# Kernel optimization log

Measured on AMD Instinct MI355X. Metric: run time of the kernel, lower is better.

## Reference

```python
import jax, jax.numpy as jnp
import numpy as np

B, S, D = 2, 2048, 4096
H, KVH, HD = 32, 8, 128          # n_heads, n_kv_heads, head_dim
N_REP = H // KVH                 # GQA repeat factor
ROPE_THETA = 10000.0
NEG = -1e9                       # finite stand-in for -inf additive mask


def setup_inputs() -> dict:
    key = jax.random.key(0)
    ks = jax.random.split(key, 5)
    x = jax.random.normal(ks[0], (B, S, D), jnp.float32)
    wq = jax.random.normal(ks[1], (D, H * HD), jnp.float32) * 0.02
    wk = jax.random.normal(ks[2], (D, KVH * HD), jnp.float32) * 0.02
    wv = jax.random.normal(ks[3], (D, KVH * HD), jnp.float32) * 0.02
    wo = jax.random.normal(ks[4], (D, D), jnp.float32) * 0.02
    # rotary frequencies: freq_cis[t, j] = exp(i * t * theta^(-2j/HD))
    inv_freq = 1.0 / (ROPE_THETA ** (jnp.arange(0, HD, 2, dtype=jnp.float32) / HD))
    angles = jnp.arange(S, dtype=jnp.float32)[:, None] * inv_freq[None, :]  # [S, HD/2]
    cos, sin = jnp.cos(angles), jnp.sin(angles)
    # causal additive mask [S, S]
    i = jnp.arange(S)
    mask = jnp.where(i[None, :] > i[:, None], NEG, 0.0).astype(jnp.float32)
    return {"x": x, "cos": cos, "sin": sin, "mask": mask,
            "wq": wq, "wk": wk, "wv": wv, "wo": wo, "start_pos": 0}


def _apply_rope(t, cos, sin):
    # t: [B, S, nH, HD] -> rotate consecutive pairs, matching view_as_complex semantics
    tp = t.reshape(*t.shape[:-1], HD // 2, 2)
    t0, t1 = tp[..., 0], tp[..., 1]
    c = cos[None, :, None, :]  # [1, S, 1, HD/2]
    s = sin[None, :, None, :]
    o0 = t0 * c - t1 * s
    o1 = t0 * s + t1 * c
    return jnp.stack([o0, o1], axis=-1).reshape(t.shape)


def reference(x, cos, sin, mask, wq, wk, wv, wo, start_pos):
    bs, seq_len, _ = x.shape
    q = (x @ wq).reshape(bs, seq_len, H, HD)
    k = (x @ wk).reshape(bs, seq_len, KVH, HD)
    v = (x @ wv).reshape(bs, seq_len, KVH, HD)
    q = _apply_rope(q, cos, sin)
    k = _apply_rope(k, cos, sin)
    # start_pos == 0 full prefill: KV cache slice [:, :start_pos+seq_len] == k, v
    # GQA: repeat_interleave kv heads (each kv head repeated N_REP times consecutively)
    k = jnp.repeat(k, N_REP, axis=2)  # [B, S, H, HD]
    v = jnp.repeat(v, N_REP, axis=2)
    attn = jnp.einsum('bqhd,bkhd->bhqk', q, k) / jnp.sqrt(jnp.float32(HD))
    attn = attn + mask[None, None, :, :]
    p = jax.nn.softmax(attn.astype(jnp.float32), axis=-1).astype(q.dtype)
    out = jnp.einsum('bhqk,bkhd->bqhd', p, v).reshape(bs, seq_len, D)
    return out @ wo
```

## Files before the change

kernel.cpp:

```cpp
#include <hip/hip_runtime.h>
#include <stdint.h>

typedef unsigned short u16;
typedef __attribute__((ext_vector_type(8))) short bf16x8;
typedef __attribute__((ext_vector_type(4))) float f32x4;

__device__ __forceinline__ u16 f2bf(float f) {
  uint32_t x = __float_as_uint(f);
  x += 0x7fffu + ((x >> 16) & 1u);
  return (u16)(x >> 16);
}
__device__ __forceinline__ float bf2f(u16 u) {
  return __uint_as_float(((uint32_t)u) << 16);
}
__device__ __forceinline__ void gload_lds16(const void* g, void* l) {
  __builtin_amdgcn_global_load_lds(
      (const __attribute__((address_space(1))) void*)g,
      (__attribute__((address_space(3))) void*)l, 16, 0, 0);
}

__device__ __forceinline__ float rope_rot(float a, int col, int srow,
                                          const float* __restrict__ cosT,
                                          const float* __restrict__ sinT) {
  float p = __shfl_xor(a, 1, 64);
  int d = (col & 127) >> 1;
  float c = cosT[srow * 64 + d];
  float sn = sinT[srow * 64 + d];
  return (col & 1) ? (p * sn + a * c) : (a * c - p * sn);
}

__global__ __launch_bounds__(256) void cvt_kernel(const float* __restrict__ x,
                                                  u16* __restrict__ y) {
  int i = blockIdx.x * 256 + threadIdx.x;
  float4 v = ((const float4*)x)[i];
  ushort4 o = make_ushort4(f2bf(v.x), f2bf(v.y), f2bf(v.z), f2bf(v.w));
  ((ushort4*)y)[i] = o;
}

__global__ __launch_bounds__(256) void transpose_cvt(const float* __restrict__ W,
                                                     u16* __restrict__ Wt,
                                                     int Kd, int Nd) {
  __shared__ float t[32][33];
  int k0 = blockIdx.y * 32, n0 = blockIdx.x * 32;
  int tx = threadIdx.x, ty = threadIdx.y;
  #pragma unroll
  for (int i = ty; i < 32; i += 8)
    t[i][tx] = W[(size_t)(k0 + i) * Nd + n0 + tx];
  __syncthreads();
  #pragma unroll
  for (int i = ty; i < 32; i += 8)
    Wt[(size_t)(n0 + i) * Kd + k0 + tx] = f2bf(t[tx][i]);
}

__global__ __launch_bounds__(256) void gemm_kv(const u16* __restrict__ A,
                                               const u16* __restrict__ Bt,
                                               u16* __restrict__ Kout,
                                               u16* __restrict__ Vt,
                                               const float* __restrict__ cosT,
                                               const float* __restrict__ sinT) {
  const int K = 4096;
  __shared__ __attribute__((aligned(16))) u16 sA[128 * 64];
  __shared__ __attribute__((aligned(16))) u16 sB[128 * 64];
  const int tid = threadIdx.x;
  const int wave = tid >> 6, lane = tid & 63;
  const int lr = lane & 15, lq = lane >> 4;
  int lin = blockIdx.y * gridDim.x + blockIdx.x;
  int cpx = (gridDim.x * gridDim.y) >> 3;
  int swz = (lin & 7) * cpx + (lin >> 3);
  const int bm = (swz >> 4) * 128, bn = (swz & 15) * 128;
  const int wm = (wave >> 1) * 64, wn = (wave & 1) * 64;
  f32x4 acc[4][4] = {};
  for (int kt = 0; kt < K; kt += 64) {
    #pragma unroll
    for (int c = 0; c < 4; ++c) {
      int chunk = wave * 4 + c;
      int eo = chunk * 512 + lane * 8;
      int r = eo >> 6, col = eo & 63;
      gload_lds16(A + (size_t)(bm + r) * K + kt + col, sA + chunk * 512);
      gload_lds16(Bt + (size_t)(bn + r) * K + kt + col, sB + chunk * 512);
    }
    __syncthreads();
    #pragma unroll
    for (int ks = 0; ks < 2; ++ks) {
      bf16x8 af[4], bfv[4];
      #pragma unroll
      for (int i = 0; i < 4; ++i)
        af[i] = *(const bf16x8*)(sA + (wm + i * 16 + lr) * 64 + ks * 32 + lq * 8);
      #pragma unroll
      for (int j = 0; j < 4; ++j)
        bfv[j] = *(const bf16x8*)(sB + (wn + j * 16 + lr) * 64 + ks * 32 + lq * 8);
      #pragma unroll
      for (int i = 0; i < 4; ++i)
        #pragma unroll
        for (int j = 0; j < 4; ++j)
          acc[i][j] = __builtin_amdgcn_mfma_f32_16x16x32_bf16(af[i], bfv[j], acc[i][j], 0, 0, 0);
    }
    __syncthreads();
  }
  #pragma unroll
  for (int i = 0; i < 4; ++i) {
    #pragma unroll
    for (int j = 0; j < 4; ++j) {
      int colg = bn + wn + j * 16 + lr;
      if (bn < 1024) {
        #pragma unroll
        for (int r = 0; r < 4; ++r) {
          int row = bm + wm + i * 16 + lq * 4 + r;
          float o = rope_rot(acc[i][j][r], colg, row & 2047, cosT, sinT);
          Kout[(size_t)row * 1024 + colg] = f2bf(o);
        }
      } else {
        int col = colg - 1024;
        int row0 = bm + wm + i * 16 + lq * 4;
        int bb = row0 >> 11, s = row0 & 2047;
        ushort4 pk = make_ushort4(f2bf(acc[i][j][0]), f2bf(acc[i][j][1]),
                                  f2bf(acc[i][j][2]), f2bf(acc[i][j][3]));
        *(ushort4*)(Vt + ((size_t)bb * 1024 + col) * 2048 + s) = pk;
      }
    }
  }
}

template <int EPI, bool ROPE>
__global__ __launch_bounds__(512, 2) void gemm256(const u16* __restrict__ A,
                                                  const u16* __restrict__ Bt,
                                                  void* __restrict__ Cout,
                                                  int M, int N, int K,
                                                  const float* __restrict__ cosT,
                                                  const float* __restrict__ sinT,
                                                  float post) {
  __shared__ __attribute__((aligned(16))) u16 sA[3][256 * 64];
  __shared__ __attribute__((aligned(16))) u16 sB[2][256 * 64];
  const int tid = threadIdx.x;
  const int wid = tid >> 6, lane = tid & 63;
  const int lr = lane & 15, lq = lane >> 4;
  const int nbn = N >> 8;
  int lin = blockIdx.y * gridDim.x + blockIdx.x;
  int cpx = (gridDim.x * gridDim.y) >> 3;
  int swz = (lin & 7) * cpx + (lin >> 3);
  const int bm = (swz / nbn) * 256, bn = (swz % nbn) * 256;
  const int wrow = (wid >> 2) * 128, wcol = (wid & 3) * 64;
  const int NK = K >> 6;

  f32x4 acc[8][4] = {};

  auto stageA = [&](int j) {
    u16* dst = &sA[j % 3][0];
    #pragma unroll
    for (int c = 0; c < 4; ++c) {
      int e = (c * 512 + tid) * 8;
      int r = e >> 6, col = e & 63;
      gload_lds16(A + (size_t)(bm + r) * K + j * 64 + (col ^ ((r & 7) << 3)), dst + e);
    }
  };
  auto stageB = [&](int j) {
    u16* dst = &sB[j & 1][0];
    #pragma unroll
    for (int c = 0; c < 4; ++c) {
      int e = (c * 512 + tid) * 8;
      int r = e >> 6, col = e & 63;
      gload_lds16(Bt + (size_t)(bn + r) * K + j * 64 + (col ^ ((r & 7) << 3)), dst + e);
    }
  };
  auto readA = [&](bf16x8* af, const u16* a_, int ks) {
    #pragma unroll
    for (int mf = 0; mf < 8; ++mf) {
      int row = wrow + mf * 16 + lr;
      af[mf] = *(const bf16x8*)(a_ + row * 64 + ((ks * 32 + lq * 8) ^ ((row & 7) << 3)));
    }
  };
  auto readB = [&](bf16x8* bfv, const u16* b_, int ks) {
    #pragma unroll
    for (int nf = 0; nf < 4; ++nf) {
      int row = wcol + nf * 16 + lr;
      bfv[nf] = *(const bf16x8*)(b_ + row * 64 + ((ks * 32 + lq * 8) ^ ((row & 7) << 3)));
    }
  };

  bf16x8 afP[8], bfP[4], afQ[8], bfQ[4];

  stageB(0); stageA(0); stageA(1); stageB(1);
  asm volatile("s_waitcnt vmcnt(8)" ::: "memory");
  asm volatile("s_barrier" ::: "memory");
  readA(afP, sA[0], 0); readB(bfP, sB[0], 0);

  for (int j = 0; j < NK; ++j) {
    const u16* a_ = sA[j % 3];
    const u16* b_ = sB[j & 1];
    const u16* an = sA[(j + 1) % 3];
    const u16* bn = sB[(j + 1) & 1];
    readA(afQ, a_, 1); readB(bfQ, b_, 1);
    if (j + 2 < NK) stageA(j + 2);
    asm volatile("s_waitcnt lgkmcnt(12)" ::: "memory");
    __builtin_amdgcn_sched_barrier(0);
    __builtin_amdgcn_s_setprio(1);
    #pragma unroll
    for (int mf = 0; mf < 8; ++mf)
      #pragma unroll
      for (int nf = 0; nf < 4; ++nf)
        acc[mf][nf] = __builtin_amdgcn_mfma_f32_16x16x32_bf16(afP[mf], bfP[nf],
                                                              acc[mf][nf], 0, 0, 0);
    __builtin_amdgcn_s_setprio(0);
    if (j + 2 < NK) asm volatile("s_waitcnt vmcnt(4)" ::: "memory");
    else            asm volatile("s_waitcnt vmcnt(0)" ::: "memory");
    asm volatile("s_barrier" ::: "memory");
    readA(afP, an, 0); readB(bfP, bn, 0);
    if (j + 2 < NK) stageB(j + 2);
    asm volatile("s_waitcnt lgkmcnt(12)" ::: "memory");
    __builtin_amdgcn_sched_barrier(0);
    __builtin_amdgcn_s_setprio(1);
    #pragma unroll
    for (int mf = 0; mf < 8; ++mf)
      #pragma unroll
      for (int nf = 0; nf < 4; ++nf)
        acc[mf][nf] = __builtin_amdgcn_mfma_f32_16x16x32_bf16(afQ[mf], bfQ[nf],
                                                              acc[mf][nf], 0, 0, 0);
    __builtin_amdgcn_s_setprio(0);
  }

  #pragma unroll
  for (int mf = 0; mf < 8; ++mf) {
    #pragma unroll
    for (int nf = 0; nf < 4; ++nf) {
      #pragma unroll
      for (int r = 0; r < 4; ++r) {
        int row = bm + wrow + mf * 16 + lq * 4 + r;
        int col = bn + wcol + nf * 16 + lr;
        if (ROPE) {
          float o = rope_rot(acc[mf][nf][r], col, row & 2047, cosT, sinT);
          ((u16*)Cout)[(size_t)row * N + col] = f2bf(o * post);
        } else if (EPI == 0) {
          ((u16*)Cout)[(size_t)row * N + col] = f2bf(acc[mf][nf][r]);
        } else {
          ((float*)Cout)[(size_t)row * N + col] = acc[mf][nf][r];
        }
      }
    }
  }
}

__global__ __launch_bounds__(256, 2) void attn_kernel(const u16* __restrict__ Q,
                                                      const u16* __restrict__ Kb,
                                                      const u16* __restrict__ Vt,
                                                      u16* __restrict__ O) {
  __shared__ __attribute__((aligned(16))) u16 sK[2][64 * 128];
  __shared__ __attribute__((aligned(16))) u16 sV[2][128 * 64];
  __shared__ __attribute__((aligned(16))) u16 sP[4][16 * 66];
  const int tid = threadIdx.x;
  const int wave = tid >> 6, lane = tid & 63;
  const int lr = lane & 15, lq = lane >> 4;
  const int p = blockIdx.x & 15;
  const int h = (blockIdx.x >> 4) & 31;
  const int b = blockIdx.x >> 9;
  const int kvh = h >> 2;
  const int qtA = p, qtB = 31 - p;
  const int q0A = qtA * 64 + wave * 16;
  const int q0B = qtB * 64 + wave * 16;
  const float NOFF = -8.0f;

  bf16x8 qfA[4], qfB[4];
  {
    const u16* qa = Q + (size_t)(b * 2048 + q0A + lr) * 4096 + h * 128 + lq * 8;
    const u16* qb = Q + (size_t)(b * 2048 + q0B + lr) * 4096 + h * 128 + lq * 8;
    #pragma unroll
    for (int ks = 0; ks < 4; ++ks) {
      qfA[ks] = *(const bf16x8*)(qa + ks * 32);
      qfB[ks] = *(const bf16x8*)(qb + ks * 32);
    }
  }

  const u16* kbase = Kb + (size_t)b * 2048 * 1024 + kvh * 128;
  const u16* vbase = Vt + (size_t)(b * 1024 + kvh * 128) * 2048;

  auto stage = [&](int kt, int bsel) {
    #pragma unroll
    for (int c = 0; c < 4; ++c) {
      int chunk = wave * 4 + c;
      int eo = chunk * 512 + lane * 8;
      int rk = eo >> 7, ck = eo & 127;
      int cks = ck ^ ((rk & 7) << 3);
      gload_lds16(kbase + (size_t)(kt * 64 + rk) * 1024 + cks,
                  (u16*)sK[bsel] + chunk * 512);
      int rv = eo >> 6, cv = eo & 63;
      int cvs = cv ^ ((rv & 7) << 3);
      gload_lds16(vbase + (size_t)rv * 2048 + kt * 64 + cvs,
                  (u16*)sV[bsel] + chunk * 512);
    }
  };

  f32x4 oA[8] = {}, oB[8] = {};
  float lA[4] = {0.f, 0.f, 0.f, 0.f}, lB[4] = {0.f, 0.f, 0.f, 0.f};

  stage(0, 0);
  __syncthreads();
  int buf = 0;
  for (int kt = 0; kt <= qtB; ++kt) {
    if (kt < qtB) stage(kt + 1, buf ^ 1);
    const u16* kb_ = sK[buf];
    const u16* vb_ = sV[buf];
    const bool doA = (kt <= qtA);

    f32x4 sAacc[4], sBacc[4];
    #pragma unroll
    for (int nf = 0; nf < 4; ++nf) {
      sAacc[nf] = (f32x4){NOFF, NOFF, NOFF, NOFF};
      sBacc[nf] = (f32x4){NOFF, NOFF, NOFF, NOFF};
    }
    __builtin_amdgcn_s_setprio(1);
    #pragma unroll
    for (int ks = 0; ks < 4; ++ks) {
      bf16x8 kf[4];
      #pragma unroll
      for (int nf = 0; nf < 4; ++nf) {
        int row = nf * 16 + lr;
        kf[nf] = *(const bf16x8*)(kb_ + row * 128 + ((ks * 32 + lq * 8) ^ ((row & 7) << 3)));
      }
      #pragma unroll
      for (int nf = 0; nf < 4; ++nf)
        sBacc[nf] = __builtin_amdgcn_mfma_f32_16x16x32_bf16(qfB[ks], kf[nf], sBacc[nf], 0, 0, 0);
      if (doA) {
        #pragma unroll
        for (int nf = 0; nf < 4; ++nf)
          sAacc[nf] = __builtin_amdgcn_mfma_f32_16x16x32_bf16(qfA[ks], kf[nf], sAacc[nf], 0, 0, 0);
      }
    }
    __builtin_amdgcn_s_setprio(0);

    auto sm_pv = [&](f32x4* sacc, float* lsum, f32x4* o, int qt, int q0) {
      float ls[4] = {0.f, 0.f, 0.f, 0.f};
      const bool diag = (kt == qt);
      #pragma unroll
      for (int nf = 0; nf < 4; ++nf)
        #pragma unroll
        for (int r = 0; r < 4; ++r) {
          float pv = __expf(sacc[nf][r]);
          if (diag) {
            int j = kt * 64 + nf * 16 + lr;
            int iq = q0 + lq * 4 + r;
            if (j > iq) pv = 0.f;
          }
          ls[r] += pv;
          sP[wave][(lq * 4 + r) * 66 + nf * 16 + lr] = f2bf(pv);
        }
      #pragma unroll
      for (int r = 0; r < 4; ++r) lsum[r] += ls[r];
      __builtin_amdgcn_s_setprio(1);
      #pragma unroll
      for (int ks = 0; ks < 2; ++ks) {
        bf16x8 pa = *(const bf16x8*)(&sP[wave][lr * 66 + ks * 32 + lq * 8]);
        #pragma unroll
        for (int df = 0; df < 8; ++df) {
          int row = df * 16 + lr;
          bf16x8 vb = *(const bf16x8*)(vb_ + row * 64 + ((ks * 32 + lq * 8) ^ ((row & 7) << 3)));
          o[df] = __builtin_amdgcn_mfma_f32_16x16x32_bf16(pa, vb, o[df], 0, 0, 0);
        }
      }
      __builtin_amdgcn_s_setprio(0);
    };

    if (doA) sm_pv(sAacc, lA, oA, qtA, q0A);
    sm_pv(sBacc, lB, oB, qtB, q0B);

    __syncthreads();
    buf ^= 1;
  }

  #pragma unroll
  for (int r = 0; r < 4; ++r) {
    float tA = lA[r], tB = lB[r];
    tA += __shfl_xor(tA, 1, 64); tB += __shfl_xor(tB, 1, 64);
    tA += __shfl_xor(tA, 2, 64); tB += __shfl_xor(tB, 2, 64);
    tA += __shfl_xor(tA, 4, 64); tB += __shfl_xor(tB, 4, 64);
    tA += __shfl_xor(tA, 8, 64); tB += __shfl_xor(tB, 8, 64);
    lA[r] = 1.f / tA; lB[r] = 1.f / tB;
  }
  #pragma unroll
  for (int df = 0; df < 8; ++df) {
    #pragma unroll
    for (int r = 0; r < 4; ++r) {
      int iqA = q0A + lq * 4 + r;
      int iqB = q0B + lq * 4 + r;
      O[(size_t)(b * 2048 + iqA) * 4096 + h * 128 + df * 16 + lr] = f2bf(oA[df][r] * lA[r]);
      O[(size_t)(b * 2048 + iqB) * 4096 + h * 128 + df * 16 + lr] = f2bf(oB[df][r] * lB[r]);
    }
  }
}

extern "C" void kernel_launch(void* const* d_in, const int* in_sizes, int n_in,
                              void* d_out, int out_size, void* d_ws, size_t ws_size,
                              hipStream_t stream) {
  (void)in_sizes; (void)n_in; (void)out_size;
  const float* x    = (const float*)d_in[0];
  const float* cosT = (const float*)d_in[1];
  const float* sinT = (const float*)d_in[2];
  const float* wq   = (const float*)d_in[4];
  const float* wk   = (const float*)d_in[5];
  const float* wv   = (const float*)d_in[6];
  const float* wo   = (const float*)d_in[7];
  float* out = (float*)d_out;
  char* ws = (char*)d_ws;

  const size_t WS_NEEDED = 201326592;
  if (ws_size < WS_NEEDED) return;

  u16* xb   = (u16*)(ws);
  u16* wqt  = (u16*)(ws + 33554432ULL);
  u16* wkvt = (u16*)(ws + 67108864ULL);
  u16* wot  = (u16*)(ws + 83886080ULL);
  u16* Qb   = (u16*)(ws + 117440512ULL);
  u16* Kbf  = (u16*)(ws + 150994944ULL);
  u16* Vt   = (u16*)(ws + 159383552ULL);
  u16* Ob   = (u16*)(ws + 167772160ULL);

  const float QSC = 0.08838834764831845f;

  cvt_kernel<<<16384, 256, 0, stream>>>(x, xb);
  transpose_cvt<<<dim3(128, 128), dim3(32, 8), 0, stream>>>(wq, wqt, 4096, 4096);
  transpose_cvt<<<dim3(32, 128),  dim3(32, 8), 0, stream>>>(wk, wkvt, 4096, 1024);
  transpose_cvt<<<dim3(32, 128),  dim3(32, 8), 0, stream>>>(wv, wkvt + 1024ULL * 4096, 4096, 1024);
  transpose_cvt<<<dim3(128, 128), dim3(32, 8), 0, stream>>>(wo, wot, 4096, 4096);

  gemm256<0, true><<<dim3(16, 16), 512, 0, stream>>>(xb, wqt, Qb, 4096, 4096, 4096,
                                                     cosT, sinT, QSC);
  gemm_kv<<<dim3(16, 32), 256, 0, stream>>>(xb, wkvt, Kbf, Vt, cosT, sinT);

  attn_kernel<<<1024, 256, 0, stream>>>(Qb, Kbf, Vt, Ob);

  gemm256<2, false><<<dim3(16, 16), 512, 0, stream>>>(Ob, wot, out, 4096, 4096, 4096,
                                                      nullptr, nullptr, 1.0f);
}
```

Before: 537.9 us.

## Software-pipeline KV GEMM with swizzled multi-buffered LDS and use exp2 softmax

Rewrites the K/V projection GEMM main loop to use a triple-buffered A and double-buffered B LDS pipeline with XOR-swizzled layout. It splits the k-tile into two halves so fragment reads for the next step overlap the MFMAs of the current one, using manual waitcnt, barrier and priority control. This is meant to hide global-load latency and LDS bank conflicts that the old single-buffer loop exposed around two syncthreads per tile. Separately, attention folds log2(e) into the Q scale and offset so the softmax can call exp2f instead of __expf. The manual vmcnt/lgkmcnt counts are fragile and raise LDS use, which may lower occupancy.

```diff
diff --git a/kernel.cpp b/kernel.cpp
--- a/kernel.cpp
+++ b/kernel.cpp
@@ -52,15 +52,16 @@
     Wt[(size_t)(n0 + i) * Kd + k0 + tx] = f2bf(t[tx][i]);
 }
 
-__global__ __launch_bounds__(256) void gemm_kv(const u16* __restrict__ A,
-                                               const u16* __restrict__ Bt,
-                                               u16* __restrict__ Kout,
-                                               u16* __restrict__ Vt,
-                                               const float* __restrict__ cosT,
-                                               const float* __restrict__ sinT) {
+__global__ __launch_bounds__(256, 2) void gemm_kv(const u16* __restrict__ A,
+                                                  const u16* __restrict__ Bt,
+                                                  u16* __restrict__ Kout,
+                                                  u16* __restrict__ Vt,
+                                                  const float* __restrict__ cosT,
+                                                  const float* __restrict__ sinT) {
   const int K = 4096;
-  __shared__ __attribute__((aligned(16))) u16 sA[128 * 64];
-  __shared__ __attribute__((aligned(16))) u16 sB[128 * 64];
+  const int NK = 64;
+  __shared__ __attribute__((aligned(16))) u16 sA[3][128 * 64];
+  __shared__ __attribute__((aligned(16))) u16 sB[2][128 * 64];
   const int tid = threadIdx.x;
   const int wave = tid >> 6, lane = tid & 63;
   const int lr = lane & 15, lq = lane >> 4;
@@ -69,34 +70,83 @@
   int swz = (lin & 7) * cpx + (lin >> 3);
   const int bm = (swz >> 4) * 128, bn = (swz & 15) * 128;
   const int wm = (wave >> 1) * 64, wn = (wave & 1) * 64;
+
   f32x4 acc[4][4] = {};
-  for (int kt = 0; kt < K; kt += 64) {
+
+  auto stageA = [&](int j) {
+    u16* dst = &sA[j % 3][0];
     #pragma unroll
     for (int c = 0; c < 4; ++c) {
-      int chunk = wave * 4 + c;
-      int eo = chunk * 512 + lane * 8;
-      int r = eo >> 6, col = eo & 63;
-      gload_lds16(A + (size_t)(bm + r) * K + kt + col, sA + chunk * 512);
-      gload_lds16(Bt + (size_t)(bn + r) * K + kt + col, sB + chunk * 512);
-    }
-    __syncthreads();
-    #pragma unroll
-    for (int ks = 0; ks < 2; ++ks) {
-      bf16x8 af[4], bfv[4];
-      #pragma unroll
-      for (int i = 0; i < 4; ++i)
-        af[i] = *(const bf16x8*)(sA + (wm + i * 16 + lr) * 64 + ks * 32 + lq * 8);
-      #pragma unroll
-      for (int j = 0; j < 4; ++j)
-        bfv[j] = *(const bf16x8*)(sB + (wn + j * 16 + lr) * 64 + ks * 32 + lq * 8);
-      #pragma unroll
-      for (int i = 0; i < 4; ++i)
-        #pragma unroll
-        for (int j = 0; j < 4; ++j)
-          acc[i][j] = __builtin_amdgcn_mfma_f32_16x16x32_bf16(af[i], bfv[j], acc[i][j], 0, 0, 0);
-    }
-    __syncthreads();
-  }
+      int e = (c * 256 + tid) * 8;
+      int r = e >> 6, col = e & 63;
+      gload_lds16(A + (size_t)(bm + r) * K + j * 64 + (col ^ ((r & 7) << 3)), dst + e);
+    }
+  };
+  auto stageB = [&](int j) {
+    u16* dst = &sB[j & 1][0];
+    #pragma unroll
+    for (int c = 0; c < 4; ++c) {
+      int e = (c * 256 + tid) * 8;
+      int r = e >> 6, col = e & 63;
+      gload_lds16(Bt + (size_t)(bn + r) * K + j * 64 + (col ^ ((r & 7) << 3)), dst + e);
+    }
+  };
+  auto readA = [&](bf16x8* af, const u16* a_, int ks) {
+    #pragma unroll
+    for (int mf = 0; mf < 4; ++mf) {
+      int row = wm + mf * 16 + lr;
+      af[mf] = *(const bf16x8*)(a_ + row * 64 + ((ks * 32 + lq * 8) ^ ((row & 7) << 3)));
+    }
+  };
+  auto readB = [&](bf16x8* bfv, const u16* b_, int ks) {
+    #pragma unroll
+    for (int nf = 0; nf < 4; ++nf) {
+      int row = wn + nf * 16 + lr;
+      bfv[nf] = *(const bf16x8*)(b_ + row * 64 + ((ks * 32 + lq * 8) ^ ((row & 7) << 3)));
+    }
+  };
+
+  bf16x8 afP[4], bfP[4], afQ[4], bfQ[4];
+
+  stageA(0); stageB(0); stageA(1); stageB(1);
+  asm volatile("s_waitcnt vmcnt(8)" ::: "memory");
+  asm volatile("s_barrier" ::: "memory");
+  readA(afP, sA[0], 0); readB(bfP, sB[0], 0);
+
+  for (int j = 0; j < NK; ++j) {
+    const u16* a_ = sA[j % 3];
+    const u16* b_ = sB[j & 1];
+    const u16* an = sA[(j + 1) % 3];
+    const u16* bn_ = sB[(j + 1) & 1];
+    readA(afQ, a_, 1); readB(bfQ, b_, 1);
+    if (j + 2 < NK) stageA(j + 2);
+    asm volatile("s_waitcnt lgkmcnt(8)" ::: "memory");
+    __builtin_amdgcn_sched_barrier(0);
+    __builtin_amdgcn_s_setprio(1);
+    #pragma unroll
+    for (int mf = 0; mf < 4; ++mf)
+      #pragma unroll
+      for (int nf = 0; nf < 4; ++nf)
+        acc[mf][nf] = __builtin_amdgcn_mfma_f32_16x16x32_bf16(afP[mf], bfP[nf],
+                                                              acc[mf][nf], 0, 0, 0);
+    __builtin_amdgcn_s_setprio(0);
+    if (j + 2 < NK) asm volatile("s_waitcnt vmcnt(4)" ::: "memory");
+    else            asm volatile("s_waitcnt vmcnt(0)" ::: "memory");
+    asm volatile("s_barrier" ::: "memory");
+    readA(afP, an, 0); readB(bfP, bn_, 0);
+    if (j + 2 < NK) stageB(j + 2);
+    asm volatile("s_waitcnt lgkmcnt(8)" ::: "memory");
+    __builtin_amdgcn_sched_barrier(0);
+    __builtin_amdgcn_s_setprio(1);
+    #pragma unroll
+    for (int mf = 0; mf < 4; ++mf)
+      #pragma unroll
+      for (int nf = 0; nf < 4; ++nf)
+        acc[mf][nf] = __builtin_amdgcn_mfma_f32_16x16x32_bf16(afQ[mf], bfQ[nf],
+                                                              acc[mf][nf], 0, 0, 0);
+    __builtin_amdgcn_s_setprio(0);
+  }
+
   #pragma unroll
   for (int i = 0; i < 4; ++i) {
     #pragma unroll
@@ -256,7 +306,7 @@
   const int qtA = p, qtB = 31 - p;
   const int q0A = qtA * 64 + wave * 16;
   const int q0B = qtB * 64 + wave * 16;
-  const float NOFF = -8.0f;
+  const float NOFF = -11.5415603f;
 
   bf16x8 qfA[4], qfB[4];
   {
@@ -333,7 +383,7 @@
       for (int nf = 0; nf < 4; ++nf)
         #pragma unroll
         for (int r = 0; r < 4; ++r) {
-          float pv = __expf(sacc[nf][r]);
+          float pv = exp2f(sacc[nf][r]);
           if (diag) {
             int j = kt * 64 + nf * 16 + lr;
             int iq = q0 + lq * 4 + r;
@@ -412,7 +462,7 @@
   u16* Vt   = (u16*)(ws + 159383552ULL);
   u16* Ob   = (u16*)(ws + 167772160ULL);
 
-  const float QSC = 0.08838834764831845f;
+  const float QSC = 0.12751746f;
 
   cvt_kernel<<<16384, 256, 0, stream>>>(x, xb);
   transpose_cvt<<<dim3(128, 128), dim3(32, 8), 0, stream>>>(wq, wqt, 4096, 4096);
```

Measured after the change: 511.8 us. -4.9%, faster.
